# Performance work log

Hardware: AMD Instinct MI355X
Metric: run time of the kernel (lower is better)

## Reference

```python
import jax, jax.numpy as jnp
import numpy as np

DIM = 512
HEADS = 8
HEAD_DIM = DIM // HEADS
SCALE = HEAD_DIM ** -0.5
LN_EPS = 1e-5


def _layernorm(t, g, b):
    mu = jnp.mean(t, axis=-1, keepdims=True)
    var = jnp.mean(jnp.square(t - mu), axis=-1, keepdims=True)
    return (t - mu) * jax.lax.rsqrt(var + LN_EPS) * g + b


def setup_inputs() -> dict:
    key = jax.random.key(0)
    ks = jax.random.split(key, 8)
    B, C, H, W = 2, DIM, 48, 48
    s = 1.0 / np.sqrt(DIM)
    return {
        "x": jax.random.normal(ks[0], (B, C, H, W), jnp.float32),
        "y": jax.random.normal(ks[1], (B, C, H, W), jnp.float32),
        # linear weights stored [in, out]
        "k_w": jax.random.uniform(ks[2], (DIM, DIM), jnp.float32, -s, s),
        "k_b": jax.random.uniform(ks[3], (DIM,), jnp.float32, -s, s),
        "qv_w": jax.random.uniform(ks[4], (DIM, 2 * DIM), jnp.float32, -s, s),
        "qv_b": jax.random.uniform(ks[5], (2 * DIM,), jnp.float32, -s, s),
        "lnx_g": jnp.ones((DIM,), jnp.float32),
        "lnx_b": jnp.zeros((DIM,), jnp.float32),
        "lny_g": jnp.ones((DIM,), jnp.float32),
        "lny_b": jnp.zeros((DIM,), jnp.float32),
    }


def _split_qv(t, qv_w, qv_b):
    B, N, C = t.shape
    qv = (t @ qv_w + qv_b).reshape(B, N, 2, HEADS, HEAD_DIM)
    qv = jnp.transpose(qv, (2, 0, 3, 1, 4))  # [2, B, h, N, d]
    return qv[0], qv[1]


def _heads(t):
    B, N, C = t.shape
    return jnp.transpose(t.reshape(B, N, HEADS, HEAD_DIM), (0, 2, 1, 3))  # [B,h,N,d]


def reference(x, y, k_w, k_b, qv_w, qv_b, lnx_g, lnx_b, lny_g, lny_b):
    B, C = x.shape[0], x.shape[1]
    xf = _layernorm(jnp.transpose(x.reshape(B, C, -1), (0, 2, 1)), lnx_g, lnx_b)  # [B,N,C]
    yf = _layernorm(jnp.transpose(y.reshape(B, C, -1), (0, 2, 1)), lny_g, lny_b)
    N = xf.shape[1]

    y_q, y_v = _split_qv(yf, qv_w, qv_b)
    x_q, x_v = _split_qv(xf, qv_w, qv_b)
    y_k = _heads(yf @ k_w + k_b)
    x_k = _heads(xf @ k_w + k_b)

    # branch 1: softmax(x_q y_k^T) x_v  -> standard [B,N,C]
    a1 = jax.nn.softmax(jnp.einsum('bhnd,bhmd->bhnm', x_q, y_k) * SCALE, axis=-1)
    xo = jnp.einsum('bhnm,bhmd->bhnd', a1, x_v)
    xo = jnp.transpose(xo, (0, 2, 1, 3)).reshape(B, N, C)

    # branch 2: faithful reproduction of torch quirk (x_k kept a leading 1-dim,
    # so the output [1,B,h,N,d].transpose(1,2).reshape(B,N,C) scrambles layout)
    a2 = jax.nn.softmax(jnp.einsum('bhnd,bhmd->bhnm', y_q, x_k) * SCALE, axis=-1)
    yo = jnp.einsum('bhnm,bhmd->bhnd', a2, y_v)  # [B,h,N,d]
    yo = jnp.transpose(yo[None], (0, 2, 1, 3, 4)).reshape(B, N, C)

    return jnp.concatenate([xo, yo], axis=0)  # [2B, N, C]
```

## Files before the change

kernel.cpp:

```cpp
#include <hip/hip_runtime.h>

#define DIM 512
#define NTOK 2304
#define HEADS 8
#define HD 64
#define LN_EPS 1e-5f
#define BNC 2359296
#define QSC 0.18033688011112042f

typedef __attribute__((ext_vector_type(8))) short short8;
typedef __attribute__((ext_vector_type(4))) short sh4;
typedef __attribute__((ext_vector_type(4))) float f32x4;

__device__ __forceinline__ short f2bf(float f) {
    union { float f; unsigned u; } x; x.f = f;
    unsigned r = (x.u + 0x7fffu + ((x.u >> 16) & 1u)) >> 16;
    return (short)(r & 0xffffu);
}
__device__ __forceinline__ unsigned fbits(float f) {
    union { float f; unsigned u; } x; x.f = f; return x.u;
}
__device__ __forceinline__ void gl2lds(const short* g, short* l) {
    __builtin_amdgcn_global_load_lds(
        (const __attribute__((address_space(1))) unsigned int*)g,
        (__attribute__((address_space(3))) unsigned int*)l, 16, 0, 0);
}

__global__ void __launch_bounds__(256)
k_stats(const float* __restrict__ x, const float* __restrict__ y,
        float* __restrict__ mu, float* __restrict__ rs) {
    __shared__ float pS[4][64], pQ[4][64];
    int bid = blockIdx.x, tid = threadIdx.x;
    int nt = bid % 36, sb = bid / 36;
    int s = sb >> 1, b = sb & 1;
    int n0 = nt * 64;
    const float* src = (s ? y : x) + (size_t)b * DIM * NTOK;
    int nl = tid & 63, part = tid >> 6;
    const float* p = src + n0 + nl;
    float sum = 0.f, sq = 0.f;
    for (int c = part * 128; c < part * 128 + 128; c++) {
        float v = p[(size_t)c * NTOK];
        sum += v; sq += v * v;
    }
    pS[part][nl] = sum; pQ[part][nl] = sq;
    __syncthreads();
    if (tid < 64) {
        float ts = pS[0][tid] + pS[1][tid] + pS[2][tid] + pS[3][tid];
        float tq = pQ[0][tid] + pQ[1][tid] + pQ[2][tid] + pQ[3][tid];
        float m = ts * (1.0f / DIM);
        float var = tq * (1.0f / DIM) - m * m;
        mu[sb * NTOK + n0 + tid] = m;
        rs[sb * NTOK + n0 + tid] = rsqrtf(var + LN_EPS);
    }
}

__global__ void k_pre(const float* __restrict__ x, const float* __restrict__ y,
                      const float* __restrict__ qv_w, const float* __restrict__ k_w,
                      const float* __restrict__ qv_b, const float* __restrict__ k_b,
                      const float* __restrict__ gx, const float* __restrict__ bx,
                      const float* __restrict__ gy, const float* __restrict__ by,
                      const float* __restrict__ mu, const float* __restrict__ rs,
                      short* __restrict__ T, short* __restrict__ Wt,
                      float* __restrict__ bias) {
    __shared__ __align__(16) float tile[64][65];
    int bkid = blockIdx.x, tid = threadIdx.x;
    if (bkid < 1152) {
        int nt = bkid % 36, ct = (bkid / 36) % 8, sb = bkid / 288;
        int s = sb >> 1, b = sb & 1;
        int n0 = nt * 64, c0 = ct * 64;
        const float* src = (s ? y : x) + (size_t)b * DIM * NTOK;
        for (int slot = tid; slot < 1024; slot += 256) {
            int r = slot >> 4, q = slot & 15;
            const float* p = src + (size_t)(c0 + r) * NTOK + n0 + q * 4;
            float4 v = *(const float4*)p;
            tile[r][q*4+0] = v.x; tile[r][q*4+1] = v.y;
            tile[r][q*4+2] = v.z; tile[r][q*4+3] = v.w;
        }
        __syncthreads();
        const float* g  = s ? gy : gx;
        const float* be = s ? by : bx;
        int nr = tid >> 2, cg = tid & 3;
        float m  = mu[sb * NTOK + n0 + nr];
        float r_ = rs[sb * NTOK + n0 + nr];
        short8 o0, o1;
        for (int i = 0; i < 8; i++) {
            int c = c0 + cg * 16 + i;
            o0[i] = f2bf((tile[cg*16+i][nr] - m) * r_ * g[c] + be[c]);
        }
        for (int i = 0; i < 8; i++) {
            int c = c0 + cg * 16 + 8 + i;
            o1[i] = f2bf((tile[cg*16+8+i][nr] - m) * r_ * g[c] + be[c]);
        }
        short* dst = T + ((size_t)sb * NTOK + n0 + nr) * DIM + c0 + cg * 16;
        *(short8*)dst = o0;
        *(short8*)(dst + 8) = o1;
        return;
    }
    int idx = bkid - 1152;
    int jt = idx % 24, ct = idx / 24;
    int j0 = jt * 64, c0 = ct * 64;
    if (ct == 0 && tid < 64) {
        int j = j0 + tid;
        bias[j] = (j < 1024) ? qv_b[j] : k_b[j - 1024];
    }
    for (int slot = tid; slot < 1024; slot += 256) {
        int r = slot >> 4, q = slot & 15;
        int c = c0 + r;
        float4 v;
        if (j0 < 1024) v = *(const float4*)(qv_w + (size_t)c * 1024 + j0 + q * 4);
        else           v = *(const float4*)(k_w  + (size_t)c * 512  + (j0 - 1024) + q * 4);
        tile[r][q*4+0] = v.x; tile[r][q*4+1] = v.y;
        tile[r][q*4+2] = v.z; tile[r][q*4+3] = v.w;
    }
    __syncthreads();
    int jr = tid >> 2, cg = tid & 3;
    short8 o0, o1;
    for (int i = 0; i < 8; i++) o0[i] = f2bf(tile[cg*16+i][jr]);
    for (int i = 0; i < 8; i++) o1[i] = f2bf(tile[cg*16+8+i][jr]);
    short* dst = Wt + (size_t)(j0 + jr) * DIM + c0 + cg * 16;
    *(short8*)dst = o0;
    *(short8*)(dst + 8) = o1;
}

__global__ void __launch_bounds__(256)
k_gemm(const short* __restrict__ T, const short* __restrict__ Wt,
       const float* __restrict__ bias, short* __restrict__ QVK,
       short* __restrict__ VT) {
    __shared__ __align__(16) short Abuf[2][128 * 64];
    __shared__ __align__(16) short Bbuf[2][128 * 64];
    int n0 = blockIdx.x * 128, j0 = blockIdx.y * 128, sb = blockIdx.z;
    int tid = threadIdx.x;
    int w = tid >> 6, l = tid & 63;
    int wr = w >> 1, wc = w & 1;
    int lrow = l & 15, quad = l >> 4;
    int r_in = (l >> 3) & 7, cc = l & 7;
    int ch = cc ^ r_in;
    int sw0 = (quad ^ (lrow & 7)) * 8;
    const short* Ab = T + (size_t)sb * NTOK * DIM;
    f32x4 acc[4][4] = {};

    #pragma unroll
    for (int inst = 0; inst < 4; inst++) {
        int R = w * 32 + inst * 8 + r_in;
        gl2lds(Ab + (size_t)(n0 + R) * 512 + 0 * 64 + ch * 8, &Abuf[0][(w * 32 + inst * 8) * 64]);
        gl2lds(Wt + (size_t)(j0 + R) * 512 + 0 * 64 + ch * 8, &Bbuf[0][(w * 32 + inst * 8) * 64]);
    }
    int cur = 0;
    for (int kk = 0; kk < 8; kk++) {
        __syncthreads();
        if (kk + 1 < 8) {
            #pragma unroll
            for (int inst = 0; inst < 4; inst++) {
                int R = w * 32 + inst * 8 + r_in;
                gl2lds(Ab + (size_t)(n0 + R) * 512 + (kk + 1) * 64 + ch * 8,
                       &Abuf[cur ^ 1][(w * 32 + inst * 8) * 64]);
                gl2lds(Wt + (size_t)(j0 + R) * 512 + (kk + 1) * 64 + ch * 8,
                       &Bbuf[cur ^ 1][(w * 32 + inst * 8) * 64]);
            }
        }
        #pragma unroll
        for (int c2 = 0; c2 < 2; c2++) {
            int off = c2 ? (sw0 ^ 32) : sw0;
            short8 af[4], bf[4];
            #pragma unroll
            for (int i = 0; i < 4; i++)
                af[i] = *(const short8*)&Abuf[cur][(wr*64 + i*16 + lrow) * 64 + off];
            #pragma unroll
            for (int j = 0; j < 4; j++)
                bf[j] = *(const short8*)&Bbuf[cur][(wc*64 + j*16 + lrow) * 64 + off];
            #pragma unroll
            for (int i = 0; i < 4; i++)
                #pragma unroll
                for (int j = 0; j < 4; j++)
                    acc[i][j] = __builtin_amdgcn_mfma_f32_16x16x32_bf16(bf[j], af[i], acc[i][j], 0, 0, 0);
        }
        cur ^= 1;
    }
    if (j0 >= 512 && j0 < 1024) {
        __syncthreads();
        short* sm = &Abuf[0][0];
        #pragma unroll
        for (int i = 0; i < 4; i++)
            #pragma unroll
            for (int j = 0; j < 4; j++) {
                int jb = wc * 64 + j * 16 + quad * 4;
                int nloc = wr * 64 + i * 16 + lrow;
                float4 bv4 = *(const float4*)&bias[j0 + jb];
                float bvs[4] = {bv4.x, bv4.y, bv4.z, bv4.w};
                #pragma unroll
                for (int reg = 0; reg < 4; reg++) {
                    int jloc = jb + reg;
                    sm[jloc * 128 + (((nloc >> 3) ^ (jloc & 15)) * 8) + (nloc & 7)]
                        = f2bf(acc[i][j][reg] + bvs[reg]);
                }
            }
        __syncthreads();
        for (int slot = tid; slot < 2048; slot += 256) {
            int row = slot >> 4, seg = slot & 15;
            short8 v = *(const short8*)&sm[row * 128 + ((seg ^ (row & 15)) * 8)];
            *(short8*)(VT + ((size_t)sb * 512 + (j0 - 512) + row) * NTOK + n0 + seg * 8) = v;
        }
    } else {
        #pragma unroll
        for (int i = 0; i < 4; i++) {
            int n = n0 + wr * 64 + i * 16 + lrow;
            #pragma unroll
            for (int j = 0; j < 4; j++) {
                int jjb = j0 + wc * 64 + j * 16 + quad * 4;
                float4 bv4 = *(const float4*)&bias[jjb];
                float bvs[4] = {bv4.x, bv4.y, bv4.z, bv4.w};
                float sc = (jjb < 512) ? QSC : 1.0f;
                sh4 pk;
                #pragma unroll
                for (int reg = 0; reg < 4; reg++)
                    pk[reg] = f2bf((acc[i][j][reg] + bvs[reg]) * sc);
                *(sh4*)&QVK[((size_t)sb * NTOK + n) * 1536 + jjb] = pk;
            }
        }
    }
}

__global__ void __launch_bounds__(256)
k_attn(const short* __restrict__ QVK, const short* __restrict__ VT,
       float* __restrict__ out, float* __restrict__ Opart,
       float* __restrict__ lbuf, int ntiles) {
    __shared__ __align__(16) short Kbuf[2][64 * 64];
    __shared__ __align__(16) short Vbuf[2][64 * 64];
    __shared__ __align__(16) short Qs[128 * 64];
    int id = blockIdx.x;
    int half = id / 576;
    int rid = id % 576;
    int xcd = rid & 7, rem = rid >> 3;
    int qt = rem % 18, yhi = rem / 18;
    int yb = yhi * 8 + xcd;
    int br = yb >> 4;
    int b  = (yb >> 3) & 1;
    int h  = yb & 7;
    int tid = threadIdx.x;
    int w = tid >> 6, l = tid & 63;
    int lrow = l & 15, quad = l >> 4;
    int r_in = (l >> 3) & 7, cc = l & 7;
    int ch = cc ^ r_in;
    int sw0 = (quad ^ (lrow & 7)) * 8;
    int n0 = qt * 128;
    int m_base = half * ntiles * 64;
    const short* Qg = QVK + ((size_t)(br * 2 + b) * NTOK) * 1536 + h * 64;
    const short* Kg = QVK + ((size_t)((1 - br) * 2 + b) * NTOK) * 1536 + 1024 + h * 64;
    const short* Vg = VT + ((size_t)(br * 2 + b) * 512 + h * 64) * NTOK;

    #pragma unroll
    for (int j = 0; j < 4; j++) {
        int R = w * 32 + j * 8 + r_in;
        gl2lds(Qg + (size_t)(n0 + R) * 1536 + ch * 8, &Qs[(w * 32 + j * 8) * 64]);
    }

    const short* KnA = Kg + (size_t)(m_base + w * 16 + r_in) * 1536 + ch * 8;
    const short* KnB = Kg + (size_t)(m_base + w * 16 + 8 + r_in) * 1536 + ch * 8;
    const short* VnA = Vg + (size_t)(w * 16 + r_in) * NTOK + m_base + ch * 8;
    const short* VnB = Vg + (size_t)(w * 16 + 8 + r_in) * NTOK + m_base + ch * 8;
    int lds_off = l * 8;

    short8 ka = *(const short8*)(KnA);
    short8 kb = *(const short8*)(KnB);
    short8 va = *(const short8*)(VnA);
    short8 vb = *(const short8*)(VnB);
    KnA += (size_t)64 * 1536; KnB += (size_t)64 * 1536;
    VnA += 64; VnB += 64;

    __syncthreads();
    short8 bq[2][2];
    #pragma unroll
    for (int qb = 0; qb < 2; qb++) {
        bq[qb][0] = *(const short8*)&Qs[(w * 32 + qb * 16 + lrow) * 64 + sw0];
        bq[qb][1] = *(const short8*)&Qs[(w * 32 + qb * 16 + lrow) * 64 + (sw0 ^ 32)];
    }
    short* Pw = &Qs[(w * 32) * 64];

    *(short8*)&Kbuf[0][(w * 16)     * 64 + lds_off] = ka;
    *(short8*)&Kbuf[0][(w * 16 + 8) * 64 + lds_off] = kb;
    *(short8*)&Vbuf[0][(w * 16)     * 64 + lds_off] = va;
    *(short8*)&Vbuf[0][(w * 16 + 8) * 64 + lds_off] = vb;
    ka = *(const short8*)(KnA);
    kb = *(const short8*)(KnB);
    va = *(const short8*)(VnA);
    vb = *(const short8*)(VnB);
    KnA += (size_t)64 * 1536; KnB += (size_t)64 * 1536;
    VnA += 64; VnB += 64;

    short8 ones;
    #pragma unroll
    for (int i = 0; i < 8; i++) ones[i] = (short)0x3F80;

    f32x4 Oacc[2][4] = {};
    f32x4 lacc[2] = {};
    int cur = 0;

    for (int mt = 0; mt < ntiles; mt++) {
        __syncthreads();
        const short* Ks = Kbuf[cur];
        const short* Vs = Vbuf[cur];

        #pragma unroll
        for (int sub = 0; sub < 4; sub++) {
            short8 ak0 = *(const short8*)&Ks[(sub * 16 + lrow) * 64 + sw0];
            short8 ak1 = *(const short8*)&Ks[(sub * 16 + lrow) * 64 + (sw0 ^ 32)];
            #pragma unroll
            for (int qb = 0; qb < 2; qb++) {
                f32x4 a = {};
                a = __builtin_amdgcn_mfma_f32_16x16x32_bf16(ak0, bq[qb][0], a, 0, 0, 0);
                a = __builtin_amdgcn_mfma_f32_16x16x32_bf16(ak1, bq[qb][1], a, 0, 0, 0);
                float p0 = __builtin_amdgcn_exp2f(a[0]), p1 = __builtin_amdgcn_exp2f(a[1]);
                float p2 = __builtin_amdgcn_exp2f(a[2]), p3 = __builtin_amdgcn_exp2f(a[3]);
                uint2 pk;
                pk.x = __builtin_amdgcn_perm(fbits(p1), fbits(p0), 0x07060302u);
                pk.y = __builtin_amdgcn_perm(fbits(p3), fbits(p2), 0x07060302u);
                *(uint2*)&Pw[(qb * 16 + lrow) * 64 +
                             (((2 * sub + (quad >> 1)) ^ (lrow & 7)) * 8) + (quad & 1) * 4] = pk;
            }
        }

        short8 ap[2][2];
        #pragma unroll
        for (int qb = 0; qb < 2; qb++) {
            ap[qb][0] = *(const short8*)&Pw[(qb * 16 + lrow) * 64 + sw0];
            ap[qb][1] = *(const short8*)&Pw[(qb * 16 + lrow) * 64 + (sw0 ^ 32)];
            lacc[qb] = __builtin_amdgcn_mfma_f32_16x16x32_bf16(ones, ap[qb][0], lacc[qb], 0, 0, 0);
            lacc[qb] = __builtin_amdgcn_mfma_f32_16x16x32_bf16(ones, ap[qb][1], lacc[qb], 0, 0, 0);
        }
        #pragma unroll
        for (int ddt = 0; ddt < 4; ddt++) {
            short8 av0 = *(const short8*)&Vs[(ddt * 16 + lrow) * 64 + sw0];
            short8 av1 = *(const short8*)&Vs[(ddt * 16 + lrow) * 64 + (sw0 ^ 32)];
            #pragma unroll
            for (int qb = 0; qb < 2; qb++) {
                Oacc[qb][ddt] = __builtin_amdgcn_mfma_f32_16x16x32_bf16(av0, ap[qb][0], Oacc[qb][ddt], 0, 0, 0);
                Oacc[qb][ddt] = __builtin_amdgcn_mfma_f32_16x16x32_bf16(av1, ap[qb][1], Oacc[qb][ddt], 0, 0, 0);
            }
        }

        if (mt + 1 < ntiles) {
            *(short8*)&Kbuf[cur ^ 1][(w * 16)     * 64 + lds_off] = ka;
            *(short8*)&Kbuf[cur ^ 1][(w * 16 + 8) * 64 + lds_off] = kb;
            *(short8*)&Vbuf[cur ^ 1][(w * 16)     * 64 + lds_off] = va;
            *(short8*)&Vbuf[cur ^ 1][(w * 16 + 8) * 64 + lds_off] = vb;
        }
        if (mt + 2 < ntiles) {
            ka = *(const short8*)(KnA);
            kb = *(const short8*)(KnB);
            va = *(const short8*)(VnA);
            vb = *(const short8*)(VnB);
        }
        KnA += (size_t)64 * 1536; KnB += (size_t)64 * 1536;
        VnA += 64; VnB += 64;
        cur ^= 1;
    }

    #pragma unroll
    for (int qb = 0; qb < 2; qb++) {
        int n = n0 + w * 32 + qb * 16 + lrow;
        if (quad == 0) lbuf[half * (32 * NTOK) + yb * NTOK + n] = lacc[qb][0];
        #pragma unroll
        for (int ddt = 0; ddt < 4; ddt++) {
            float4 o;
            o.x = Oacc[qb][ddt][0];
            o.y = Oacc[qb][ddt][1];
            o.z = Oacc[qb][ddt][2];
            o.w = Oacc[qb][ddt][3];
            if (half == 0) {
                if (br == 0)
                    *(float4*)&out[((size_t)b * NTOK + n) * 512 + h * 64 + ddt * 16 + quad * 4] = o;
                else
                    *(float4*)&out[(size_t)BNC + ((size_t)(h * 2 + b) * NTOK + n) * 64 + ddt * 16 + quad * 4] = o;
            } else {
                *(float4*)&Opart[(size_t)(half - 1) * 4718592 +
                                 ((size_t)yb * NTOK + n) * 64 + ddt * 16 + quad * 4] = o;
            }
        }
    }
}

__global__ void __launch_bounds__(256)
k_norm(float* __restrict__ out, const float* __restrict__ Opart,
       const float* __restrict__ lbuf, int ns) {
    int i = blockIdx.x * 256 + threadIdx.x;
    int o = i * 4;
    int yb, n, d;
    if (o < BNC) {
        int b = o / (NTOK * 512);
        int r = o % (NTOK * 512);
        n = r >> 9;
        int c = r & 511;
        d = c & 63;
        yb = b * 8 + (c >> 6);
    } else {
        int o2 = o - BNC;
        int hb = o2 / (NTOK * 64);
        n = (o2 >> 6) % NTOK;
        d = o2 & 63;
        yb = 16 + (hb & 1) * 8 + (hb >> 1);
    }
    int li = yb * NTOK + n;
    float lsum = 0.f;
    for (int k = 0; k < ns; k++) lsum += lbuf[k * (32 * NTOK) + li];
    float linv = 1.f / lsum;
    float4 a = *(const float4*)&out[o];
    for (int k = 1; k < ns; k++) {
        float4 q = *(const float4*)&Opart[(size_t)(k - 1) * 4718592 + (size_t)li * 64 + d];
        a.x += q.x; a.y += q.y; a.z += q.z; a.w += q.w;
    }
    a.x *= linv; a.y *= linv; a.z *= linv; a.w *= linv;
    *(float4*)&out[o] = a;
}

extern "C" void kernel_launch(void* const* d_in, const int* in_sizes, int n_in,
                              void* d_out, int out_size, void* d_ws, size_t ws_size,
                              hipStream_t stream) {
    const float* x     = (const float*)d_in[0];
    const float* y     = (const float*)d_in[1];
    const float* k_w   = (const float*)d_in[2];
    const float* k_b   = (const float*)d_in[3];
    const float* qv_w  = (const float*)d_in[4];
    const float* qv_b  = (const float*)d_in[5];
    const float* lnx_g = (const float*)d_in[6];
    const float* lnx_b = (const float*)d_in[7];
    const float* lny_g = (const float*)d_in[8];
    const float* lny_b = (const float*)d_in[9];
    float* out = (float*)d_out;

    char* ws = (char*)d_ws;
    float* bias = (float*)ws;
    float* mu   = (float*)(ws + 6144);
    float* rs   = (float*)(ws + 43008);
    short* T    = (short*)(ws + 79872);
    short* Wt   = (short*)(ws + 9517056);
    short* QVK  = (short*)(ws + 11089920);
    short* VT   = (short*)(ws + 39401472);
    float* lbuf = (float*)(ws + 48838656);
    float* Opart= (float*)(ws + 50018304);

    int ns = (ws_size >= 50018304ull + 3ull * 18874368ull) ? 4 : 2;
    int ntiles = 36 / ns;

    k_stats<<<144, 256, 0, stream>>>(x, y, mu, rs);
    k_pre  <<<1344, 256, 0, stream>>>(x, y, qv_w, k_w, qv_b, k_b,
                                      lnx_g, lnx_b, lny_g, lny_b, mu, rs, T, Wt, bias);
    k_gemm <<<dim3(18, 12, 4), 256, 0, stream>>>(T, Wt, bias, QVK, VT);
    k_attn <<<576 * ns, 256, 0, stream>>>(QVK, VT, out, Opart, lbuf, ntiles);
    k_norm <<<4608, 256, 0, stream>>>(out, Opart, lbuf, ns);
}
```

Baseline: 206.8 us.

## Load K/V fragments directly from global memory, dropping LDS staging and barriers

```diff
diff --git a/kernel.cpp b/kernel.cpp
--- a/kernel.cpp
+++ b/kernel.cpp
@@ -224,9 +224,7 @@
 k_attn(const short* __restrict__ QVK, const short* __restrict__ VT,
        float* __restrict__ out, float* __restrict__ Opart,
        float* __restrict__ lbuf, int ntiles) {
-    __shared__ __align__(16) short Kbuf[2][64 * 64];
-    __shared__ __align__(16) short Vbuf[2][64 * 64];
-    __shared__ __align__(16) short Qs[128 * 64];
+    __shared__ __align__(16) short Ps[4][32 * 64];
     int id = blockIdx.x;
     int half = id / 576;
     int rid = id % 576;
@@ -239,8 +237,6 @@
     int tid = threadIdx.x;
     int w = tid >> 6, l = tid & 63;
     int lrow = l & 15, quad = l >> 4;
-    int r_in = (l >> 3) & 7, cc = l & 7;
-    int ch = cc ^ r_in;
     int sw0 = (quad ^ (lrow & 7)) * 8;
     int n0 = qt * 128;
     int m_base = half * ntiles * 64;
@@ -248,44 +244,17 @@
     const short* Kg = QVK + ((size_t)((1 - br) * 2 + b) * NTOK) * 1536 + 1024 + h * 64;
     const short* Vg = VT + ((size_t)(br * 2 + b) * 512 + h * 64) * NTOK;
 
-    #pragma unroll
-    for (int j = 0; j < 4; j++) {
-        int R = w * 32 + j * 8 + r_in;
-        gl2lds(Qg + (size_t)(n0 + R) * 1536 + ch * 8, &Qs[(w * 32 + j * 8) * 64]);
-    }
-
-    const short* KnA = Kg + (size_t)(m_base + w * 16 + r_in) * 1536 + ch * 8;
-    const short* KnB = Kg + (size_t)(m_base + w * 16 + 8 + r_in) * 1536 + ch * 8;
-    const short* VnA = Vg + (size_t)(w * 16 + r_in) * NTOK + m_base + ch * 8;
-    const short* VnB = Vg + (size_t)(w * 16 + 8 + r_in) * NTOK + m_base + ch * 8;
-    int lds_off = l * 8;
-
-    short8 ka = *(const short8*)(KnA);
-    short8 kb = *(const short8*)(KnB);
-    short8 va = *(const short8*)(VnA);
-    short8 vb = *(const short8*)(VnB);
-    KnA += (size_t)64 * 1536; KnB += (size_t)64 * 1536;
-    VnA += 64; VnB += 64;
-
-    __syncthreads();
     short8 bq[2][2];
     #pragma unroll
     for (int qb = 0; qb < 2; qb++) {
-        bq[qb][0] = *(const short8*)&Qs[(w * 32 + qb * 16 + lrow) * 64 + sw0];
-        bq[qb][1] = *(const short8*)&Qs[(w * 32 + qb * 16 + lrow) * 64 + (sw0 ^ 32)];
-    }
-    short* Pw = &Qs[(w * 32) * 64];
-
-    *(short8*)&Kbuf[0][(w * 16)     * 64 + lds_off] = ka;
-    *(short8*)&Kbuf[0][(w * 16 + 8) * 64 + lds_off] = kb;
-    *(short8*)&Vbuf[0][(w * 16)     * 64 + lds_off] = va;
-    *(short8*)&Vbuf[0][(w * 16 + 8) * 64 + lds_off] = vb;
-    ka = *(const short8*)(KnA);
-    kb = *(const short8*)(KnB);
-    va = *(const short8*)(VnA);
-    vb = *(const short8*)(VnB);
-    KnA += (size_t)64 * 1536; KnB += (size_t)64 * 1536;
-    VnA += 64; VnB += 64;
+        const short* qrow = Qg + (size_t)(n0 + w * 32 + qb * 16 + lrow) * 1536 + quad * 8;
+        bq[qb][0] = *(const short8*)(qrow);
+        bq[qb][1] = *(const short8*)(qrow + 32);
+    }
+    short* Pw = Ps[w];
+
+    const short* Kp = Kg + (size_t)(m_base + lrow) * 1536 + quad * 8;
+    const short* Vp = Vg + (size_t)lrow * NTOK + m_base + quad * 8;
 
     short8 ones;
     #pragma unroll
@@ -293,17 +262,13 @@
 
     f32x4 Oacc[2][4] = {};
     f32x4 lacc[2] = {};
-    int cur = 0;
 
     for (int mt = 0; mt < ntiles; mt++) {
-        __syncthreads();
-        const short* Ks = Kbuf[cur];
-        const short* Vs = Vbuf[cur];
-
         #pragma unroll
         for (int sub = 0; sub < 4; sub++) {
-            short8 ak0 = *(const short8*)&Ks[(sub * 16 + lrow) * 64 + sw0];
-            short8 ak1 = *(const short8*)&Ks[(sub * 16 + lrow) * 64 + (sw0 ^ 32)];
+            const short* krow = Kp + (size_t)(sub * 16) * 1536;
+            short8 ak0 = *(const short8*)(krow);
+            short8 ak1 = *(const short8*)(krow + 32);
             #pragma unroll
             for (int qb = 0; qb < 2; qb++) {
                 f32x4 a = {};
@@ -329,30 +294,17 @@
         }
         #pragma unroll
         for (int ddt = 0; ddt < 4; ddt++) {
-            short8 av0 = *(const short8*)&Vs[(ddt * 16 + lrow) * 64 + sw0];
-            short8 av1 = *(const short8*)&Vs[(ddt * 16 + lrow) * 64 + (sw0 ^ 32)];
+            const short* vrow = Vp + (size_t)(ddt * 16) * NTOK;
+            short8 av0 = *(const short8*)(vrow);
+            short8 av1 = *(const short8*)(vrow + 32);
             #pragma unroll
             for (int qb = 0; qb < 2; qb++) {
                 Oacc[qb][ddt] = __builtin_amdgcn_mfma_f32_16x16x32_bf16(av0, ap[qb][0], Oacc[qb][ddt], 0, 0, 0);
                 Oacc[qb][ddt] = __builtin_amdgcn_mfma_f32_16x16x32_bf16(av1, ap[qb][1], Oacc[qb][ddt], 0, 0, 0);
             }
         }
-
-        if (mt + 1 < ntiles) {
-            *(short8*)&Kbuf[cur ^ 1][(w * 16)     * 64 + lds_off] = ka;
-            *(short8*)&Kbuf[cur ^ 1][(w * 16 + 8) * 64 + lds_off] = kb;
-            *(short8*)&Vbuf[cur ^ 1][(w * 16)     * 64 + lds_off] = va;
-            *(short8*)&Vbuf[cur ^ 1][(w * 16 + 8) * 64 + lds_off] = vb;
-        }
-        if (mt + 2 < ntiles) {
-            ka = *(const short8*)(KnA);
-            kb = *(const short8*)(KnB);
-            va = *(const short8*)(VnA);
-            vb = *(const short8*)(VnB);
-        }
-        KnA += (size_t)64 * 1536; KnB += (size_t)64 * 1536;
-        VnA += 64; VnB += 64;
-        cur ^= 1;
+        Kp += (size_t)64 * 1536;
+        Vp += 64;
     }
 
     #pragma unroll
```

Result: slower. 302.3 us (+46.2%).
